# Kernel optimization log

Measured on AMD Instinct MI355X. Metric: run time of the kernel, lower is better.

The kernel has to match this reference:

```python
import jax, jax.numpy as jnp
import numpy as np

B, S, D = 4, 2048, 1024
H, Dh = 16, 64


def setup_inputs() -> dict:
    key = jax.random.key(0)
    ks = jax.random.split(key, 9)
    s_in = 1.0 / np.sqrt(D)
    inp = {
        "key": jax.random.normal(ks[0], (B, S, D), jnp.float32),
        "value": jax.random.normal(ks[1], (B, S, D), jnp.float32),
        "query": jax.random.normal(ks[2], (B, S, D), jnp.float32),
        # Linear weights stored as [in, out] (math-equivalent to torch W.T)
        "Wq": jax.random.uniform(ks[3], (D, H * Dh), jnp.float32, -s_in, s_in),
        "bq": jax.random.uniform(ks[4], (H * Dh,), jnp.float32, -s_in, s_in),
        "Wk": jax.random.uniform(ks[5], (D, H * Dh), jnp.float32, -s_in, s_in),
        "bk": jax.random.uniform(ks[6], (H * Dh,), jnp.float32, -s_in, s_in),
        "Wv": jax.random.uniform(ks[7], (D, H * Dh), jnp.float32, -s_in, s_in),
        "bv": jax.random.uniform(ks[8], (H * Dh,), jnp.float32, -s_in, s_in),
    }
    return inp


def reference(key, value, query, Wq, bq, Wk, bk, Wv, bv):
    b, s, _ = key.shape
    # projections -> [B, H, S, Dh]
    q = (query @ Wq + bq).reshape(b, s, H, Dh).transpose(0, 2, 1, 3)
    k = (key @ Wk + bk).reshape(b, s, H, Dh).transpose(0, 2, 1, 3)
    v = (value @ Wv + bv).reshape(b, s, H, Dh).transpose(0, 2, 1, 3)
    scores = jnp.einsum("bhqd,bhkd->bhqk", q, k) / np.sqrt(Dh).astype(np.float32)
    p = jax.nn.softmax(scores, axis=-1)
    out = jnp.einsum("bhqk,bhkd->bhqd", p, v)  # [B, H, S, Dh]
    return out.transpose(0, 2, 1, 3).reshape(b, s, H * Dh)
```

## Files before the change

### kernel.cpp

```cpp
#include <hip/hip_runtime.h>

typedef __bf16 bf16;
typedef __bf16 bf16x8 __attribute__((ext_vector_type(8)));
typedef __bf16 bf16x4 __attribute__((ext_vector_type(4)));
typedef _Float16 f16x4 __attribute__((ext_vector_type(4)));
typedef _Float16 f16x8 __attribute__((ext_vector_type(8)));
typedef __fp16 h16x2 __attribute__((ext_vector_type(2)));
typedef float  f32x4  __attribute__((ext_vector_type(4)));
typedef float  f32x16 __attribute__((ext_vector_type(16)));
typedef unsigned int uint2v __attribute__((ext_vector_type(2)));
typedef unsigned int uint4v __attribute__((ext_vector_type(4)));

#define LOG2E 1.44269504088896340736f
#define SCQ (0.125f * LOG2E)

__device__ __forceinline__ void async16(const void* g, void* l) {
  __builtin_amdgcn_global_load_lds(
      (const __attribute__((address_space(1))) unsigned int*)g,
      (__attribute__((address_space(3))) unsigned int*)l, 16, 0, 0);
}

__device__ __forceinline__ f32x4 mfma_bf16(bf16x8 a, bf16x8 b, f32x4 c) {
  return __builtin_amdgcn_mfma_f32_16x16x32_bf16(a, b, c, 0, 0, 0);
}
__device__ __forceinline__ f32x16 mfma32_bf16(bf16x8 a, bf16x8 b, f32x16 c) {
  return __builtin_amdgcn_mfma_f32_32x32x16_bf16(a, b, c, 0, 0, 0);
}
__device__ __forceinline__ f32x16 mfma32x16_f16(f16x8 a, f16x8 b, f32x16 c) {
  return __builtin_amdgcn_mfma_f32_32x32x16_f16(a, b, c, 0, 0, 0);
}

__global__ __launch_bounds__(256) void prep(const float* __restrict__ q,
                                            const float* __restrict__ k,
                                            const float* __restrict__ v,
                                            const float* __restrict__ W0,
                                            const float* __restrict__ W1,
                                            const float* __restrict__ W2,
                                            bf16* __restrict__ actb,
                                            bf16* __restrict__ Wt) {
  __shared__ float t[64 * 69];
  const int z = blockIdx.y, tid = threadIdx.x;
  if (blockIdx.x < 4096) {
    const float* in = z == 0 ? q : (z == 1 ? k : v);
    bf16* o = actb + (size_t)z * 8388608;
    int i = blockIdx.x * 256 + tid;
    const float4* p = (const float4*)in;
    float4 a = p[i * 2], c = p[i * 2 + 1];
    bf16x8 r;
    r[0] = (bf16)a.x; r[1] = (bf16)a.y; r[2] = (bf16)a.z; r[3] = (bf16)a.w;
    r[4] = (bf16)c.x; r[5] = (bf16)c.y; r[6] = (bf16)c.z; r[7] = (bf16)c.w;
    ((bf16x8*)o)[i] = r;
  } else {
    const float* W = z == 0 ? W0 : (z == 1 ? W1 : W2);
    bf16* O = Wt + (size_t)z * (1024 * 1024);
    int lin = blockIdx.x - 4096;
    int k0 = (lin & 15) * 64, n0 = (lin >> 4) * 64;
    int r0 = tid >> 4, c0 = (tid & 15) * 4;
#pragma unroll
    for (int rr = 0; rr < 4; rr++) {
      int kk = r0 + rr * 16;
      float4 vv = *(const float4*)(W + (k0 + kk) * 1024 + n0 + c0);
      t[kk * 69 + c0 + 0] = vv.x; t[kk * 69 + c0 + 1] = vv.y;
      t[kk * 69 + c0 + 2] = vv.z; t[kk * 69 + c0 + 3] = vv.w;
    }
    __syncthreads();
#pragma unroll
    for (int rr = 0; rr < 4; rr++) {
      int n = r0 + rr * 16;
      bf16x4 o;
#pragma unroll
      for (int j = 0; j < 4; j++) o[j] = (bf16)t[(c0 + j) * 69 + n];
      *(bf16x4*)(O + (n0 + n) * 1024 + k0 + c0) = o;
    }
  }
}

__global__ __launch_bounds__(256, 3) void gemm_qkv(const bf16* __restrict__ Act,
                                                   const bf16* __restrict__ Wt,
                                                   const float* __restrict__ b0,
                                                   const float* __restrict__ b1,
                                                   const float* __restrict__ b2,
                                                   bf16* __restrict__ qo,
                                                   bf16* __restrict__ ko,
                                                   _Float16* __restrict__ vf) {
  __shared__ bf16 smem[16384];
  bf16* sA = smem;
  bf16* sB = smem + 8192;
  const int tid = threadIdx.x;
  const int wave = tid >> 6, lane = tid & 63;
  const int quad = lane >> 4, l15 = lane & 15;
  const int z = blockIdx.z;
  const int m0 = blockIdx.x * 128, n0 = blockIdx.y * 128;
  const bf16* A = Act + (size_t)z * 8388608;
  const bf16* Bt = Wt + (size_t)z * 1048576;
  const float* bias = z == 0 ? b0 : (z == 1 ? b1 : b2);

  const bf16* ap[4]; const bf16* bp[4]; int lo[4];
#pragma unroll
  for (int i = 0; i < 4; i++) {
    int g = wave * 256 + i * 64 + lane;
    int row = g >> 3, jl = (g & 7) ^ (row & 7);
    ap[i] = A + (m0 + row) * 1024 + jl * 8;
    bp[i] = Bt + (n0 + row) * 1024 + jl * 8;
    lo[i] = (wave * 256 + i * 64) * 8;
  }
  const int wm = (wave & 1) * 64, wn = (wave >> 1) * 64;
  f32x4 acc[4][4] = {};

  for (int kt = 0; kt < 16; kt++) {
    const int ko_ = kt * 64;
#pragma unroll
    for (int i = 0; i < 4; i++) async16(ap[i] + ko_, sA + lo[i]);
#pragma unroll
    for (int i = 0; i < 4; i++) async16(bp[i] + ko_, sB + lo[i]);
    __syncthreads();
#pragma unroll
    for (int ks = 0; ks < 2; ks++) {
      bf16x8 af[4], bv[4];
#pragma unroll
      for (int mt = 0; mt < 4; mt++) {
        int m = wm + mt * 16 + l15;
        int ph = (ks * 4 + quad) ^ (m & 7);
        af[mt] = *(const bf16x8*)(sA + m * 64 + ph * 8);
      }
#pragma unroll
      for (int nt = 0; nt < 4; nt++) {
        int n = wn + nt * 16 + l15;
        int ph = (ks * 4 + quad) ^ (n & 7);
        bv[nt] = *(const bf16x8*)(sB + n * 64 + ph * 8);
      }
#pragma unroll
      for (int mt = 0; mt < 4; mt++)
#pragma unroll
        for (int nt = 0; nt < 4; nt++)
          acc[mt][nt] = mfma_bf16(af[mt], bv[nt], acc[mt][nt]);
    }
    __syncthreads();
  }

  if (z != 2) {
    bf16* O = z == 0 ? qo : ko;
    const float sc = z == 0 ? SCQ : 1.0f;
#pragma unroll
    for (int nt = 0; nt < 4; nt++) {
      int n = n0 + wn + nt * 16 + l15;
      float bc = bias[n];
#pragma unroll
      for (int mt = 0; mt < 4; mt++)
#pragma unroll
        for (int r = 0; r < 4; r++) {
          int m = m0 + wm + mt * 16 + quad * 4 + r;
          O[m * 1024 + n] = (bf16)((acc[mt][nt][r] + bc) * sc);
        }
    }
  } else {
    const int b = m0 >> 11, s0 = m0 & 2047;
    const int kvb = s0 >> 7;
    const int mtg0 = (wave & 1) * 4;
    const int hl = quad >> 1, jb = (quad & 1) * 4;
#pragma unroll
    for (int nt = 0; nt < 4; nt++) {
      int n = n0 + wn + nt * 16;
      int hh = n >> 6, db = (n >> 5) & 1;
      int lanep = hl * 32 + (n & 31) + l15;
      float bc = bias[n + l15];
#pragma unroll
      for (int mt = 0; mt < 4; mt++) {
        int fi = (mtg0 + mt) * 2 + db;
        f16x4 pk;
#pragma unroll
        for (int r = 0; r < 4; r++) pk[r] = (_Float16)(acc[mt][nt][r] + bc);
        size_t off = ((((size_t)(b * 16 + hh) * 16 + kvb) * 16 + fi) * 512)
                     + lanep * 8 + jb;
        *(f16x4*)(vf + off) = pk;
      }
    }
  }
}

__global__ __launch_bounds__(256, 3) void attn(const bf16* __restrict__ Q,
                                               const bf16* __restrict__ K,
                                               const _Float16* __restrict__ VF,
                                               float* __restrict__ Out) {
  __shared__ bf16 sQ[8192];
  __shared__ bf16 sK[8192];
  __shared__ _Float16 sV[8192];
  const int tid = threadIdx.x;
  const int wave = tid >> 6, lane = tid & 63;
  const int l31 = lane & 31, hl = lane >> 5;
  const int q0 = blockIdx.x * 128, hh = blockIdx.y, b = blockIdx.z;
  const bf16* Kbase = K + (size_t)(b * 2048) * 1024 + hh * 64;
  const _Float16* Vbase = VF + (size_t)(b * 16 + hh) * 131072;

#pragma unroll
  for (int i = 0; i < 4; i++) {
    int g = i * 256 + tid;
    int row = g >> 3, jl = (g & 7) ^ (row & 7);
    async16(Q + (size_t)(b * 2048 + q0 + row) * 1024 + hh * 64 + jl * 8, sQ + g * 8);
    async16(Kbase + (size_t)row * 1024 + jl * 8, sK + g * 8);
    async16(Vbase + g * 8, sV + g * 8);
  }
  __syncthreads();

  bf16x8 qf[4];
  {
    int rowq = wave * 32 + l31, rx = rowq & 7;
#pragma unroll
    for (int i = 0; i < 4; i++)
      qf[i] = *(const bf16x8*)(sQ + rowq * 64 + ((2 * i + hl) ^ rx) * 8);
  }

  f32x16 oacc[2] = {};
  float ls = 0.f;

  for (int kvb = 0; kvb < 16; kvb++) {
#pragma unroll
    for (int t32 = 0; t32 < 4; t32++) {
      int rowk = t32 * 32 + l31, rx = rowk & 7;
      const bf16* kr = sK + rowk * 64;
      f32x16 st = {};
#pragma unroll
      for (int i = 0; i < 4; i++) {
        bf16x8 kf = *(const bf16x8*)(kr + ((2 * i + hl) ^ rx) * 8);
        st = mfma32_bf16(kf, qf[i], st);
      }
      unsigned int dw[8];
      float ps = 0.f;
#pragma unroll
      for (int s = 0; s < 4; s++) {
        float p0 = __builtin_amdgcn_exp2f(st[4 * s + 0]);
        float p1 = __builtin_amdgcn_exp2f(st[4 * s + 1]);
        float p2 = __builtin_amdgcn_exp2f(st[4 * s + 2]);
        float p3 = __builtin_amdgcn_exp2f(st[4 * s + 3]);
        ps += (p0 + p1) + (p2 + p3);
        dw[2 * s]     = __builtin_bit_cast(unsigned int,
                          __builtin_amdgcn_cvt_pkrtz(p0, p1));
        dw[2 * s + 1] = __builtin_bit_cast(unsigned int,
                          __builtin_amdgcn_cvt_pkrtz(p2, p3));
      }
      ls += ps;
#pragma unroll
      for (int u = 0; u < 2; u++) {
        uint2v rA = __builtin_amdgcn_permlane32_swap(dw[4 * u + 0],
                                                     dw[4 * u + 2], false, false);
        uint2v rB = __builtin_amdgcn_permlane32_swap(dw[4 * u + 1],
                                                     dw[4 * u + 3], false, false);
        uint4v uu;
        uu[0] = rA[0]; uu[1] = rB[0]; uu[2] = rA[1]; uu[3] = rB[1];
        f16x8 pfrag = __builtin_bit_cast(f16x8, uu);
#pragma unroll
        for (int db = 0; db < 2; db++) {
          f16x8 va = *(const f16x8*)(sV + ((t32 * 4 + u * 2 + db) * 64 + lane) * 8);
          oacc[db] = mfma32x16_f16(va, pfrag, oacc[db]);
        }
      }
    }
    __syncthreads();
    if (kvb < 15) {
      int kn = (kvb + 1) * 128;
#pragma unroll
      for (int i = 0; i < 4; i++) {
        int g = i * 256 + tid;
        int row = g >> 3, jl = (g & 7) ^ (row & 7);
        async16(Kbase + (size_t)(kn + row) * 1024 + jl * 8, sK + g * 8);
        async16(Vbase + (kvb + 1) * 8192 + g * 8, sV + g * 8);
      }
      __syncthreads();
    }
  }

  ls += __shfl_xor(ls, 32);
  float inv = 1.f / ls;
  int qrow = b * 2048 + q0 + wave * 32 + l31;
  float* orow = Out + (size_t)qrow * 1024 + hh * 64;
#pragma unroll
  for (int db = 0; db < 2; db++)
#pragma unroll
    for (int rg = 0; rg < 4; rg++) {
      float4 v;
      v.x = oacc[db][4 * rg + 0] * inv;
      v.y = oacc[db][4 * rg + 1] * inv;
      v.z = oacc[db][4 * rg + 2] * inv;
      v.w = oacc[db][4 * rg + 3] * inv;
      *(float4*)(orow + db * 32 + rg * 8 + 4 * hl) = v;
    }
}

extern "C" void kernel_launch(void* const* d_in, const int* in_sizes, int n_in,
                              void* d_out, int out_size, void* d_ws, size_t ws_size,
                              hipStream_t stream) {
  const float* key   = (const float*)d_in[0];
  const float* value = (const float*)d_in[1];
  const float* query = (const float*)d_in[2];
  const float* Wq = (const float*)d_in[3];
  const float* bq = (const float*)d_in[4];
  const float* Wk = (const float*)d_in[5];
  const float* bk = (const float*)d_in[6];
  const float* Wv = (const float*)d_in[7];
  const float* bv = (const float*)d_in[8];
  float* out = (float*)d_out;

  char* ws = (char*)d_ws;
  bf16* actb   = (bf16*)(ws);
  bf16* wt     = (bf16*)(ws + 50331648);
  bf16* qo     = (bf16*)(ws + 56623104);
  bf16* ko     = (bf16*)(ws + 73400320);
  _Float16* vf = (_Float16*)(ws + 90177536);
  (void)in_sizes; (void)n_in; (void)out_size; (void)ws_size;

  prep<<<dim3(4352, 3), 256, 0, stream>>>(query, key, value, Wq, Wk, Wv, actb, wt);
  gemm_qkv<<<dim3(64, 8, 3), 256, 0, stream>>>(actb, wt, bq, bk, bv, qo, ko, vf);
  attn<<<dim3(16, 16, 4), 256, 0, stream>>>(qo, ko, vf, out);
}
```

Measured before the change: 290.8 us.

## Double-buffer K/V tiles in LDS to overlap loads with attention compute

Splits the single 128-row K/V LDS tile into two 64-row ping-pong buffers and issues the async global-to-LDS load for the next tile before computing on the current one. This is meant to hide global memory latency that was previously fully exposed by the load-then-sync sequence. It halves the tile size, doubling the number of iterations and barriers, and relies on async load completion being covered by the barrier.

```diff
diff --git a/kernel.cpp b/kernel.cpp
--- a/kernel.cpp
+++ b/kernel.cpp
@@ -183,8 +183,8 @@
                                                const _Float16* __restrict__ VF,
                                                float* __restrict__ Out) {
   __shared__ bf16 sQ[8192];
-  __shared__ bf16 sK[8192];
-  __shared__ _Float16 sV[8192];
+  __shared__ bf16 sK0[4096], sK1[4096];
+  __shared__ _Float16 sV0[4096], sV1[4096];
   const int tid = threadIdx.x;
   const int wave = tid >> 6, lane = tid & 63;
   const int l31 = lane & 31, hl = lane >> 5;
@@ -192,14 +192,26 @@
   const bf16* Kbase = K + (size_t)(b * 2048) * 1024 + hh * 64;
   const _Float16* Vbase = VF + (size_t)(b * 16 + hh) * 131072;
 
+  const int g0 = tid, g1 = 256 + tid;
+  const int r0s = g0 >> 3, j0s = (g0 & 7) ^ (r0s & 7);
+  const int r1s = g1 >> 3, j1s = (g1 & 7) ^ (r1s & 7);
+  const bf16* kst0 = Kbase + (size_t)r0s * 1024 + j0s * 8;
+  const bf16* kst1 = Kbase + (size_t)r1s * 1024 + j1s * 8;
+
+  auto stageKV = [&](int t, bf16* sk, _Float16* sv) {
+    async16(kst0 + (size_t)t * 65536, sk + g0 * 8);
+    async16(kst1 + (size_t)t * 65536, sk + g1 * 8);
+    async16(Vbase + t * 4096 + g0 * 8, sv + g0 * 8);
+    async16(Vbase + t * 4096 + g1 * 8, sv + g1 * 8);
+  };
+
 #pragma unroll
   for (int i = 0; i < 4; i++) {
     int g = i * 256 + tid;
     int row = g >> 3, jl = (g & 7) ^ (row & 7);
     async16(Q + (size_t)(b * 2048 + q0 + row) * 1024 + hh * 64 + jl * 8, sQ + g * 8);
-    async16(Kbase + (size_t)row * 1024 + jl * 8, sK + g * 8);
-    async16(Vbase + g * 8, sV + g * 8);
-  }
+  }
+  stageKV(0, sK0, sV0);
   __syncthreads();
 
   bf16x8 qf[4];
@@ -213,11 +225,11 @@
   f32x16 oacc[2] = {};
   float ls = 0.f;
 
-  for (int kvb = 0; kvb < 16; kvb++) {
-#pragma unroll
-    for (int t32 = 0; t32 < 4; t32++) {
+  auto computeT = [&](const bf16* sk, const _Float16* sv) {
+#pragma unroll
+    for (int t32 = 0; t32 < 2; t32++) {
       int rowk = t32 * 32 + l31, rx = rowk & 7;
-      const bf16* kr = sK + rowk * 64;
+      const bf16* kr = sk + rowk * 64;
       f32x16 st = {};
 #pragma unroll
       for (int i = 0; i < 4; i++) {
@@ -250,23 +262,21 @@
         f16x8 pfrag = __builtin_bit_cast(f16x8, uu);
 #pragma unroll
         for (int db = 0; db < 2; db++) {
-          f16x8 va = *(const f16x8*)(sV + ((t32 * 4 + u * 2 + db) * 64 + lane) * 8);
+          f16x8 va = *(const f16x8*)(sv + ((t32 * 4 + u * 2 + db) * 64 + lane) * 8);
           oacc[db] = mfma32x16_f16(va, pfrag, oacc[db]);
         }
       }
     }
-    __syncthreads();
-    if (kvb < 15) {
-      int kn = (kvb + 1) * 128;
-#pragma unroll
-      for (int i = 0; i < 4; i++) {
-        int g = i * 256 + tid;
-        int row = g >> 3, jl = (g & 7) ^ (row & 7);
-        async16(Kbase + (size_t)(kn + row) * 1024 + jl * 8, sK + g * 8);
-        async16(Vbase + (kvb + 1) * 8192 + g * 8, sV + g * 8);
-      }
-      __syncthreads();
-    }
+  };
+
+#pragma unroll 1
+  for (int t = 0; t < 32; t += 2) {
+    stageKV(t + 1, sK1, sV1);
+    computeT(sK0, sV0);
+    __syncthreads();
+    if (t + 2 < 32) stageKV(t + 2, sK0, sV0);
+    computeT(sK1, sV1);
+    __syncthreads();
   }
 
   ls += __shfl_xor(ls, 32);
```

Result: no change. 290.0 us (-0.3%).
